# Kernel tuning notes

Hardware: AMD Instinct MI355X
Metric: run time of the kernel (lower is better)

The kernel has to match this reference:

```python
import jax, jax.numpy as jnp
import numpy as np

N_EMBD = 768
N_HEAD = 12
EPS = 1e-5

def setup_inputs() -> dict:
    key = jax.random.key(0)
    ks = jax.random.split(key, 13)
    C = N_EMBD
    s = lambda n: 1.0 / np.sqrt(n)
    return {
        "x":      jax.random.normal(ks[0], (2, 2048, C), dtype=jnp.float32),
        "ln1_w":  jnp.ones((C,), jnp.float32),
        "ln1_b":  jnp.zeros((C,), jnp.float32),
        "w_qkv":  jax.random.normal(ks[1], (C, 3 * C), dtype=jnp.float32) * s(C),
        "b_qkv":  jnp.zeros((3 * C,), jnp.float32),
        "w_proj": jax.random.normal(ks[2], (C, C), dtype=jnp.float32) * s(C),
        "b_proj": jnp.zeros((C,), jnp.float32),
        "ln2_w":  jnp.ones((C,), jnp.float32),
        "ln2_b":  jnp.zeros((C,), jnp.float32),
        "w_fc1":  jax.random.normal(ks[3], (C, 4 * C), dtype=jnp.float32) * s(C),
        "b_fc1":  jnp.zeros((4 * C,), jnp.float32),
        "w_fc2":  jax.random.normal(ks[4], (4 * C, C), dtype=jnp.float32) * s(4 * C),
        "b_fc2":  jnp.zeros((C,), jnp.float32),
    }

def _layernorm(x, w, b):
    mu = jnp.mean(x, axis=-1, keepdims=True)
    var = jnp.mean(jnp.square(x - mu), axis=-1, keepdims=True)
    return (x - mu) * jax.lax.rsqrt(var + EPS) * w + b

def reference(x, ln1_w, ln1_b, w_qkv, b_qkv, w_proj, b_proj,
              ln2_w, ln2_b, w_fc1, b_fc1, w_fc2, b_fc2):
    B, T, C = x.shape
    H = N_HEAD
    hd = C // H
    # --- attention branch ---
    h = _layernorm(x, ln1_w, ln1_b)
    qkv = h @ w_qkv + b_qkv                                  # [B,T,3C]
    q, k, v = jnp.split(qkv, 3, axis=-1)
    q = q.reshape(B, T, H, hd).transpose(0, 2, 1, 3)          # [B,H,T,hd]
    k = k.reshape(B, T, H, hd).transpose(0, 2, 1, 3)
    v = v.reshape(B, T, H, hd).transpose(0, 2, 1, 3)
    att = jnp.einsum('bhqd,bhkd->bhqk', q, k) * (1.0 / np.sqrt(hd))
    causal = jnp.tril(jnp.ones((T, T), dtype=bool))
    att = jnp.where(causal, att, -jnp.inf)
    att = jax.nn.softmax(att, axis=-1)
    y = jnp.einsum('bhqk,bhkd->bhqd', att, v)                 # [B,H,T,hd]
    y = y.transpose(0, 2, 1, 3).reshape(B, T, C)
    x = x + (y @ w_proj + b_proj)
    # --- MLP branch (dropout = identity in eval) ---
    h = _layernorm(x, ln2_w, ln2_b)
    h = jax.nn.gelu(h @ w_fc1 + b_fc1, approximate=False)
    x = x + (h @ w_fc2 + b_fc2)
    return x
```

## Files before the change

### kernel.cpp

```cpp
#include <hip/hip_runtime.h>
#include <math.h>

typedef __attribute__((ext_vector_type(8))) short short8;
typedef __attribute__((ext_vector_type(4))) float floatx4;

__device__ __forceinline__ unsigned short f2bf(float f) {
    union { float f; unsigned u; } v; v.f = f;
    unsigned r = v.u + 0x7fffu + ((v.u >> 16) & 1u);
    return (unsigned short)(r >> 16);
}

__device__ __forceinline__ float bf2f(unsigned short h) {
    union { unsigned u; float f; } v; v.u = ((unsigned)h) << 16; return v.f;
}

__device__ __forceinline__ float fexp2(float x) {
#if __has_builtin(__builtin_amdgcn_exp2f)
    return __builtin_amdgcn_exp2f(x);
#else
    return __expf(x * 0.69314718056f);
#endif
}

__device__ __forceinline__ void gload16(const unsigned short* g, unsigned short* l) {
    __builtin_amdgcn_global_load_lds(
        (const __attribute__((address_space(1))) unsigned int*)g,
        (__attribute__((address_space(3))) unsigned int*)l, 16, 0, 0);
}

__global__ __launch_bounds__(256) void ln_kernel(const float* __restrict__ x,
                                                 const float* __restrict__ w,
                                                 const float* __restrict__ b,
                                                 unsigned short* __restrict__ o) {
    int row = blockIdx.x, tid = threadIdx.x;
    const float* xr = x + (size_t)row * 768;
    float v0 = xr[tid], v1 = xr[tid + 256], v2 = xr[tid + 512];
    float s = v0 + v1 + v2, ss = v0 * v0 + v1 * v1 + v2 * v2;
#pragma unroll
    for (int o_ = 32; o_; o_ >>= 1) { s += __shfl_xor(s, o_); ss += __shfl_xor(ss, o_); }
    __shared__ float red[8];
    if ((tid & 63) == 0) { red[tid >> 6] = s; red[(tid >> 6) + 4] = ss; }
    __syncthreads();
    s = red[0] + red[1] + red[2] + red[3];
    ss = red[4] + red[5] + red[6] + red[7];
    float mu = s * (1.f / 768.f);
    float var = ss * (1.f / 768.f) - mu * mu;
    float inv = rsqrtf(var + 1e-5f);
    unsigned short* orow = o + (size_t)row * 768;
    orow[tid]       = f2bf((v0 - mu) * inv * w[tid]       + b[tid]);
    orow[tid + 256] = f2bf((v1 - mu) * inv * w[tid + 256] + b[tid + 256]);
    orow[tid + 512] = f2bf((v2 - mu) * inv * w[tid + 512] + b[tid + 512]);
}

__global__ __launch_bounds__(256) void wt_kernel(const float* __restrict__ w,
                                                 unsigned short* __restrict__ wt,
                                                 int K, int N) {
    __shared__ float t[32][33];
    int n0 = blockIdx.x * 32, k0 = blockIdx.y * 32;
    int tx = threadIdx.x & 31, ty = threadIdx.x >> 5;
#pragma unroll
    for (int i = 0; i < 32; i += 8)
        t[ty + i][tx] = w[(size_t)(k0 + ty + i) * N + n0 + tx];
    __syncthreads();
#pragma unroll
    for (int i = 0; i < 32; i += 8)
        wt[(size_t)(n0 + ty + i) * K + k0 + tx] = f2bf(t[tx][ty + i]);
}

template <int EPI>
__global__ __launch_bounds__(256) void gemm_kernel(
    const unsigned short* __restrict__ A, const unsigned short* __restrict__ Bt,
    const float* __restrict__ bias, const float* __restrict__ resid,
    float* __restrict__ fout, unsigned short* __restrict__ o0,
    unsigned short* __restrict__ o1, unsigned short* __restrict__ o2,
    int K, int Kcnt) {
    __shared__ unsigned short Al[2][128 * 32];
    __shared__ unsigned short Bl[2][128 * 32];
    int tid = threadIdx.x, lane = tid & 63, w = tid >> 6;
    int wm = w >> 1, wn = w & 1;
    int nwg = (int)(gridDim.x * gridDim.y);
    int wgid = (int)(blockIdx.y * gridDim.x + blockIdx.x);
    int logical = (wgid & 7) * (nwg >> 3) + (wgid >> 3);
    int by = logical & 31, bx = logical >> 5;
    int m0 = by * 128;
    int n0, kof = 0, chunk = 0;
    if (EPI == 4) {
        n0 = (bx % 6) * 128;
        chunk = bx / 6;
        kof = chunk * 768;
    } else {
        n0 = bx * 128;
    }
    int lr = lane & 15, lk = (lane >> 4) << 3;

    int srow = w * 32 + (lane >> 2);
    int sko = (lane & 3) << 3;
    const unsigned short* Ab = A + (size_t)(m0 + srow) * K + kof + sko;
    const unsigned short* Bb = Bt + (size_t)(n0 + srow) * K + kof + sko;

    floatx4 acc[4][4];
#pragma unroll
    for (int i = 0; i < 4; i++)
#pragma unroll
        for (int j = 0; j < 4; j++) acc[i][j] = (floatx4){0.f, 0.f, 0.f, 0.f};

    int nk = Kcnt >> 5;
    auto stage = [&](int buf, int t) {
        int k0 = t << 5;
        unsigned short* Alp = &Al[buf][(w * 32) * 32];
        unsigned short* Blp = &Bl[buf][(w * 32) * 32];
        gload16(Ab + k0, Alp);
        gload16(Ab + 16 * K + k0, Alp + 16 * 32);
        gload16(Bb + k0, Blp);
        gload16(Bb + 16 * K + k0, Blp + 16 * 32);
    };

    stage(0, 0);
    for (int t = 0; t < nk; t++) {
        int cur = t & 1;
        __syncthreads();
        if (t + 1 < nk) stage(cur ^ 1, t + 1);
        short8 af[4], bfr[4];
#pragma unroll
        for (int mt = 0; mt < 4; mt++) af[mt] = *(short8*)&Al[cur][(wm * 64 + mt * 16 + lr) * 32 + lk];
#pragma unroll
        for (int nt = 0; nt < 4; nt++) bfr[nt] = *(short8*)&Bl[cur][(wn * 64 + nt * 16 + lr) * 32 + lk];
#pragma unroll
        for (int mt = 0; mt < 4; mt++)
#pragma unroll
            for (int nt = 0; nt < 4; nt++)
                acc[mt][nt] = __builtin_amdgcn_mfma_f32_16x16x32_bf16(af[mt], bfr[nt], acc[mt][nt], 0, 0, 0);
    }

    int mb = m0 + wm * 64, nb = n0 + wn * 64;
    int sec = 0;
    if (EPI == 0) sec = n0 / 768;
#pragma unroll
    for (int mt = 0; mt < 4; mt++)
#pragma unroll
        for (int nt = 0; nt < 4; nt++)
#pragma unroll
            for (int r = 0; r < 4; r++) {
                int mrow = mb + mt * 16 + ((lane >> 4) << 2) + r;
                int ncol = nb + nt * 16 + lr;
                float val = acc[mt][nt][r];
                if (EPI != 4) val += bias[ncol];
                if (EPI == 0) {
                    int f = ncol - sec * 768;
                    int h = f >> 6, d = f & 63;
                    int bb = mrow >> 11, t = mrow & 2047;
                    if (sec == 0)
                        o0[((size_t)(bb * 12 + h) * 2048 + t) * 64 + d] = f2bf(val * 0.1803368801f);
                    else if (sec == 1)
                        o1[((size_t)(bb * 12 + h) * 2048 + t) * 64 + d] = f2bf(val);
                    else
                        o2[((size_t)(bb * 12 + h) * 64 + d) * 2048 + t] = f2bf(val);
                } else if (EPI == 1) {
                    fout[(size_t)mrow * 768 + ncol] = val + resid[(size_t)mrow * 768 + ncol];
                } else if (EPI == 2) {
                    float g = 0.5f * val * (1.f + erff(val * 0.70710678118f));
                    o0[(size_t)mrow * 3072 + ncol] = f2bf(g);
                } else if (EPI == 3) {
                    fout[(size_t)mrow * 768 + ncol] = val + resid[(size_t)mrow * 768 + ncol];
                } else {
                    unsigned short* op = (chunk == 0) ? o0 : (chunk == 1) ? o1
                                       : (chunk == 2) ? o2 : (unsigned short*)fout;
                    op[(size_t)mrow * 768 + ncol] = f2bf(val);
                }
            }
}

__global__ __launch_bounds__(256) void fc2_combine(
    const unsigned short* __restrict__ p0, const unsigned short* __restrict__ p1,
    const unsigned short* __restrict__ p2, const unsigned short* __restrict__ p3,
    const float* __restrict__ bias, const float* __restrict__ resid,
    float* __restrict__ out) {
    int i = blockIdx.x * 256 + threadIdx.x;
    size_t base = (size_t)i * 8;
    int col = (int)(base % 768);
    short8 a0 = *(const short8*)&p0[base];
    short8 a1 = *(const short8*)&p1[base];
    short8 a2 = *(const short8*)&p2[base];
    short8 a3 = *(const short8*)&p3[base];
#pragma unroll
    for (int j = 0; j < 8; j++) {
        float s = bf2f((unsigned short)a0[j]) + bf2f((unsigned short)a1[j]) +
                  bf2f((unsigned short)a2[j]) + bf2f((unsigned short)a3[j]);
        out[base + j] = s + bias[col + j] + resid[base + j];
    }
}

__global__ __launch_bounds__(256) void attn_kernel(const unsigned short* __restrict__ q_s,
                                                   const unsigned short* __restrict__ k_s,
                                                   const unsigned short* __restrict__ v_t,
                                                   unsigned short* __restrict__ y,
                                                   unsigned short* __restrict__ opart,
                                                   float* __restrict__ lpart) {
    __shared__ unsigned short KVs[2][8192];
    __shared__ unsigned short Pls[4][32][72];
    const int T = 2048, H = 12;
    int tid = threadIdx.x, lane = tid & 63, w = tid >> 6;
    int xx = (int)blockIdx.x;
    int bq, c;
    if (xx < 16)      { c = 0; bq = xx; }
    else if (xx < 28) { c = 1; bq = xx - 12; }
    else if (xx < 36) { c = 2; bq = xx - 20; }
    else              { c = 3; bq = xx - 24; }
    int bh = blockIdx.y;
    int bi = bh / H, hh = bh - bi * H;
    const unsigned short* qp = q_s + (size_t)bh * T * 64;
    const unsigned short* kp = k_s + (size_t)bh * T * 64;
    const unsigned short* vp = v_t + (size_t)bh * 64 * T;
    int wq0 = bq * 128 + w * 32;
    int lr = lane & 15, lk8 = (lane >> 4) << 3, hi = lane >> 4;
    int nt_blk = 2 * bq + 2;
    int t0 = c * 8;
    int t1 = t0 + 8 < nt_blk ? t0 + 8 : nt_blk;

    unsigned short (*Pl)[72] = Pls[w];

    int srow = tid >> 3, ssl = tid & 7;

    auto stage = [&](int buf, int t) {
        int kv0 = t * 64;
        unsigned short* base = &KVs[buf][(tid >> 6) * 512];
#pragma unroll
        for (int h = 0; h < 2; h++) {
            int r = srow + h * 32;
            int ss = ssl ^ (r & 7);
            gload16(kp + (size_t)(kv0 + r) * 64 + ss * 8, base + h * 2048);
            gload16(vp + (size_t)r * T + kv0 + ss * 8, base + 4096 + h * 2048);
        }
    };

    short8 aq[2][2];
#pragma unroll
    for (int mt = 0; mt < 2; mt++)
#pragma unroll
        for (int kf = 0; kf < 2; kf++)
            aq[mt][kf] = *(const short8*)&qp[(size_t)(wq0 + mt * 16 + lr) * 64 + kf * 32 + lk8];

    floatx4 yacc[2][4];
    float lacc[2][4];
#pragma unroll
    for (int i = 0; i < 2; i++)
#pragma unroll
        for (int j = 0; j < 4; j++) {
            yacc[i][j] = (floatx4){0.f, 0.f, 0.f, 0.f};
            lacc[i][j] = 0.f;
        }

    stage(0, t0);
    __syncthreads();

    for (int t = t0; t < t1; t++) {
        int cur = (t - t0) & 1;
        if (t + 1 < t1) stage(cur ^ 1, t + 1);
        int kv0 = t * 64;
        if (kv0 <= wq0 + 31) {
            const unsigned short* Kt = &KVs[cur][0];
            const unsigned short* Vt = &KVs[cur][4096];
            floatx4 sacc[2][4];
#pragma unroll
            for (int i = 0; i < 2; i++)
#pragma unroll
                for (int j = 0; j < 4; j++) sacc[i][j] = (floatx4){0.f, 0.f, 0.f, 0.f};
#pragma unroll
            for (int kf = 0; kf < 2; kf++) {
                int sl = ((kf << 2) | hi) ^ (lr & 7);
                short8 bk[4];
#pragma unroll
                for (int nt = 0; nt < 4; nt++)
                    bk[nt] = *(const short8*)&Kt[(nt * 16 + lr) * 64 + sl * 8];
#pragma unroll
                for (int mt = 0; mt < 2; mt++)
#pragma unroll
                    for (int nt = 0; nt < 4; nt++)
                        sacc[mt][nt] = __builtin_amdgcn_mfma_f32_16x16x32_bf16(aq[mt][kf], bk[nt], sacc[mt][nt], 0, 0, 0);
            }
            bool full = (kv0 + 63 <= wq0);
#pragma unroll
            for (int mt = 0; mt < 2; mt++)
#pragma unroll
                for (int r = 0; r < 4; r++) {
                    int qg = wq0 + mt * 16 + (hi << 2) + r;
                    int prow = mt * 16 + (hi << 2) + r;
#pragma unroll
                    for (int nt = 0; nt < 4; nt++) {
                        float sv = sacc[mt][nt][r];
                        if (!full) {
                            int kvg = kv0 + nt * 16 + lr;
                            sv = (kvg <= qg) ? sv : -1e30f;
                        }
                        float p = fexp2(sv);
                        lacc[mt][r] += p;
                        Pl[prow][nt * 16 + lr] = f2bf(p);
                    }
                }
#pragma unroll
            for (int kf = 0; kf < 2; kf++) {
                int sl = ((kf << 2) | hi) ^ (lr & 7);
                short8 pa[2], bv[4];
#pragma unroll
                for (int mt = 0; mt < 2; mt++) pa[mt] = *(short8*)&Pl[mt * 16 + lr][kf * 32 + lk8];
#pragma unroll
                for (int nt = 0; nt < 4; nt++)
                    bv[nt] = *(const short8*)&Vt[(nt * 16 + lr) * 64 + sl * 8];
#pragma unroll
                for (int mt = 0; mt < 2; mt++)
#pragma unroll
                    for (int nt = 0; nt < 4; nt++)
                        yacc[mt][nt] = __builtin_amdgcn_mfma_f32_16x16x32_bf16(pa[mt], bv[nt], yacc[mt][nt], 0, 0, 0);
            }
        }
        __syncthreads();
    }

    if (bq < 4) {
#pragma unroll
        for (int mt = 0; mt < 2; mt++)
#pragma unroll
            for (int r = 0; r < 4; r++) {
                float l = lacc[mt][r];
                l += __shfl_xor(l, 1);
                l += __shfl_xor(l, 2);
                l += __shfl_xor(l, 4);
                l += __shfl_xor(l, 8);
                float inv = 1.f / l;
                int qg = wq0 + mt * 16 + (hi << 2) + r;
#pragma unroll
                for (int nt = 0; nt < 4; nt++)
                    y[((size_t)(bi * T + qg)) * 768 + hh * 64 + nt * 16 + lr] = f2bf(yacc[mt][nt][r] * inv);
            }
    } else {
        int g = bq >> 2, rr = bq & 3;
        int base = (g == 1) ? 2 * rr : (g == 2) ? 8 + 3 * rr : 20 + 4 * rr;
        int slab = bh * 36 + base + c;
        unsigned short* op = opart + (size_t)slab * 8192;
        float* lp = lpart + (size_t)slab * 128;
#pragma unroll
        for (int mt = 0; mt < 2; mt++)
#pragma unroll
            for (int r = 0; r < 4; r++) {
                float l = lacc[mt][r];
                l += __shfl_xor(l, 1);
                l += __shfl_xor(l, 2);
                l += __shfl_xor(l, 4);
                l += __shfl_xor(l, 8);
                int wrow = w * 32 + mt * 16 + (hi << 2) + r;
                if (lr == 0) lp[wrow] = l;
#pragma unroll
                for (int nt = 0; nt < 4; nt++)
                    op[(size_t)wrow * 64 + nt * 16 + lr] = f2bf(yacc[mt][nt][r]);
            }
    }
}

__global__ __launch_bounds__(256) void attn_combine(const unsigned short* __restrict__ opart,
                                                    const float* __restrict__ lpart,
                                                    unsigned short* __restrict__ y) {
    const int T = 2048, H = 12;
    int bq = 4 + (int)blockIdx.x;
    int bh = blockIdx.y;
    int bi = bh / H, hh = bh - bi * H;
    int nchunk = (bq >> 2) + 1;
    int g = bq >> 2, rr = bq & 3;
    int base = (g == 1) ? 2 * rr : (g == 2) ? 8 + 3 * rr : 20 + 4 * rr;
    int tid = threadIdx.x;
    int row = tid >> 1, cb = (tid & 1) * 32;

    float l = 0.f;
    for (int c = 0; c < nchunk; c++) l += lpart[(size_t)(bh * 36 + base + c) * 128 + row];
    float inv = 1.f / l;

    float s[32];
#pragma unroll
    for (int j = 0; j < 32; j++) s[j] = 0.f;
    for (int c = 0; c < nchunk; c++) {
        const unsigned short* op = opart + ((size_t)(bh * 36 + base + c) * 128 + row) * 64 + cb;
#pragma unroll
        for (int v = 0; v < 4; v++) {
            short8 ob = *(const short8*)&op[v * 8];
#pragma unroll
            for (int j = 0; j < 8; j++) s[v * 8 + j] += bf2f((unsigned short)ob[j]);
        }
    }
    int qg = bq * 128 + row;
    unsigned short* yr = y + ((size_t)(bi * T + qg)) * 768 + hh * 64 + cb;
#pragma unroll
    for (int v = 0; v < 4; v++) {
        short8 ob;
#pragma unroll
        for (int j = 0; j < 8; j++) ob[j] = (short)f2bf(s[v * 8 + j] * inv);
        *(short8*)&yr[v * 8] = ob;
    }
}

extern "C" void kernel_launch(void* const* d_in, const int* in_sizes, int n_in,
                              void* d_out, int out_size, void* d_ws, size_t ws_size,
                              hipStream_t stream) {
    const float* x    = (const float*)d_in[0];
    const float* ln1w = (const float*)d_in[1];
    const float* ln1b = (const float*)d_in[2];
    const float* wqkv = (const float*)d_in[3];
    const float* bqkv = (const float*)d_in[4];
    const float* wproj= (const float*)d_in[5];
    const float* bproj= (const float*)d_in[6];
    const float* ln2w = (const float*)d_in[7];
    const float* ln2b = (const float*)d_in[8];
    const float* wfc1 = (const float*)d_in[9];
    const float* bfc1 = (const float*)d_in[10];
    const float* wfc2 = (const float*)d_in[11];
    const float* bfc2 = (const float*)d_in[12];
    float* out = (float*)d_out;

    char* ws = (char*)d_ws;
    size_t off = 0;
    auto alloc = [&](size_t bytes) { void* p = ws + off; off += (bytes + 255) & ~(size_t)255; return p; };

    const size_t MT = 4096;
    unsigned short* wqkv_t = (unsigned short*)alloc(2304 * 768 * 2);
    unsigned short* wproj_t= (unsigned short*)alloc(768 * 768 * 2);
    unsigned short* wfc1_t = (unsigned short*)alloc(3072 * 768 * 2);
    unsigned short* wfc2_t = (unsigned short*)alloc(768 * 3072 * 2);
    unsigned short* h12    = (unsigned short*)alloc(MT * 768 * 2);
    float*          x1     = (float*)alloc(MT * 768 * 4);
    unsigned short* qs     = (unsigned short*)alloc(MT * 768 * 2);
    unsigned short* ks     = (unsigned short*)alloc(MT * 768 * 2);
    unsigned short* vt     = (unsigned short*)alloc(MT * 768 * 2);
    unsigned short* yb     = (unsigned short*)alloc(MT * 768 * 2);
    unsigned short* hm     = qs;
    unsigned short* opart  = (unsigned short*)alloc(24 * 36 * 8192 * 2);
    float*          lpart  = (float*)alloc(24 * 36 * 128 * 4);

    unsigned short* p0 = (unsigned short*)ws;
    unsigned short* p1 = opart;
    unsigned short* p2 = (unsigned short*)((char*)opart + (size_t)MT * 768 * 2);
    unsigned short* p3 = h12;

    wt_kernel<<<dim3(2304 / 32, 768 / 32), 256, 0, stream>>>(wqkv, wqkv_t, 768, 2304);
    wt_kernel<<<dim3(768 / 32, 768 / 32), 256, 0, stream>>>(wproj, wproj_t, 768, 768);
    wt_kernel<<<dim3(3072 / 32, 768 / 32), 256, 0, stream>>>(wfc1, wfc1_t, 768, 3072);
    wt_kernel<<<dim3(768 / 32, 3072 / 32), 256, 0, stream>>>(wfc2, wfc2_t, 3072, 768);

    ln_kernel<<<4096, 256, 0, stream>>>(x, ln1w, ln1b, h12);
    gemm_kernel<0><<<dim3(18, 32), 256, 0, stream>>>(h12, wqkv_t, bqkv, nullptr, nullptr, qs, ks, vt, 768, 768);
    attn_kernel<<<dim3(40, 24), 256, 0, stream>>>(qs, ks, vt, yb, opart, lpart);
    attn_combine<<<dim3(12, 24), 256, 0, stream>>>(opart, lpart, yb);
    gemm_kernel<1><<<dim3(6, 32), 256, 0, stream>>>(yb, wproj_t, bproj, x, x1, nullptr, nullptr, nullptr, 768, 768);
    ln_kernel<<<4096, 256, 0, stream>>>(x1, ln2w, ln2b, h12);
    gemm_kernel<2><<<dim3(24, 32), 256, 0, stream>>>(h12, wfc1_t, bfc1, nullptr, nullptr, hm, nullptr, nullptr, 768, 768);
    gemm_kernel<4><<<dim3(24, 32), 256, 0, stream>>>(hm, wfc2_t, nullptr, nullptr, (float*)p3, p0, p1, p2, 3072, 768);
    fc2_combine<<<dim3(1536), 256, 0, stream>>>(p0, p1, p2, p3, bfc2, x1, out);
}
```

Baseline: 215.8 us.

## Use 256x128 tiles with 512-thread blocks for QKV, FC1 and split-K FC2 GEMMs

```diff
diff --git a/kernel.cpp b/kernel.cpp
--- a/kernel.cpp
+++ b/kernel.cpp
@@ -82,21 +82,13 @@
     int wgid = (int)(blockIdx.y * gridDim.x + blockIdx.x);
     int logical = (wgid & 7) * (nwg >> 3) + (wgid >> 3);
     int by = logical & 31, bx = logical >> 5;
-    int m0 = by * 128;
-    int n0, kof = 0, chunk = 0;
-    if (EPI == 4) {
-        n0 = (bx % 6) * 128;
-        chunk = bx / 6;
-        kof = chunk * 768;
-    } else {
-        n0 = bx * 128;
-    }
+    int m0 = by * 128, n0 = bx * 128;
     int lr = lane & 15, lk = (lane >> 4) << 3;
 
     int srow = w * 32 + (lane >> 2);
     int sko = (lane & 3) << 3;
-    const unsigned short* Ab = A + (size_t)(m0 + srow) * K + kof + sko;
-    const unsigned short* Bb = Bt + (size_t)(n0 + srow) * K + kof + sko;
+    const unsigned short* Ab = A + (size_t)(m0 + srow) * K + sko;
+    const unsigned short* Bb = Bt + (size_t)(n0 + srow) * K + sko;
 
     floatx4 acc[4][4];
 #pragma unroll
@@ -113,6 +105,84 @@
         gload16(Ab + 16 * K + k0, Alp + 16 * 32);
         gload16(Bb + k0, Blp);
         gload16(Bb + 16 * K + k0, Blp + 16 * 32);
+    };
+
+    stage(0, 0);
+    for (int t = 0; t < nk; t++) {
+        int cur = t & 1;
+        __syncthreads();
+        if (t + 1 < nk) stage(cur ^ 1, t + 1);
+        short8 af[4], bfr[4];
+#pragma unroll
+        for (int mt = 0; mt < 4; mt++) af[mt] = *(short8*)&Al[cur][(wm * 64 + mt * 16 + lr) * 32 + lk];
+#pragma unroll
+        for (int nt = 0; nt < 4; nt++) bfr[nt] = *(short8*)&Bl[cur][(wn * 64 + nt * 16 + lr) * 32 + lk];
+#pragma unroll
+        for (int mt = 0; mt < 4; mt++)
+#pragma unroll
+            for (int nt = 0; nt < 4; nt++)
+                acc[mt][nt] = __builtin_amdgcn_mfma_f32_16x16x32_bf16(af[mt], bfr[nt], acc[mt][nt], 0, 0, 0);
+    }
+
+    int mb = m0 + wm * 64, nb = n0 + wn * 64;
+#pragma unroll
+    for (int mt = 0; mt < 4; mt++)
+#pragma unroll
+        for (int nt = 0; nt < 4; nt++)
+#pragma unroll
+            for (int r = 0; r < 4; r++) {
+                int mrow = mb + mt * 16 + ((lane >> 4) << 2) + r;
+                int ncol = nb + nt * 16 + lr;
+                float val = acc[mt][nt][r] + bias[ncol];
+                fout[(size_t)mrow * 768 + ncol] = val + resid[(size_t)mrow * 768 + ncol];
+            }
+}
+
+template <int EPI>
+__global__ __launch_bounds__(512) void gemm256_kernel(
+    const unsigned short* __restrict__ A, const unsigned short* __restrict__ Bt,
+    const float* __restrict__ bias, const float* __restrict__ resid,
+    float* __restrict__ fout, unsigned short* __restrict__ o0,
+    unsigned short* __restrict__ o1, unsigned short* __restrict__ o2,
+    int K, int Kcnt) {
+    __shared__ unsigned short Al[2][256 * 32];
+    __shared__ unsigned short Bl[2][128 * 32];
+    int tid = threadIdx.x, lane = tid & 63, w = tid >> 6;
+    int wm = w >> 1, wn = w & 1;
+    int nwg = (int)(gridDim.x * gridDim.y);
+    int wgid = (int)(blockIdx.y * gridDim.x + blockIdx.x);
+    int logical = (wgid & 7) * (nwg >> 3) + (wgid >> 3);
+    int my = (int)gridDim.y;
+    int by = logical % my, bx = logical / my;
+    int m0 = by * 256;
+    int n0, kof = 0, chunk = 0;
+    if (EPI == 4) {
+        n0 = (bx % 6) * 128;
+        chunk = bx / 6;
+        kof = chunk * 768;
+    } else {
+        n0 = bx * 128;
+    }
+    int lr = lane & 15, lk = (lane >> 4) << 3;
+
+    int arow = w * 32 + (lane >> 2);
+    int brow = w * 16 + (lane >> 2);
+    int sko = (lane & 3) << 3;
+    const unsigned short* Ab = A + (size_t)(m0 + arow) * K + kof + sko;
+    const unsigned short* Bb = Bt + (size_t)(n0 + brow) * K + kof + sko;
+
+    floatx4 acc[4][4];
+#pragma unroll
+    for (int i = 0; i < 4; i++)
+#pragma unroll
+        for (int j = 0; j < 4; j++) acc[i][j] = (floatx4){0.f, 0.f, 0.f, 0.f};
+
+    int nk = Kcnt >> 5;
+    auto stage = [&](int buf, int t) {
+        int k0 = t << 5;
+        gload16(Ab + k0, &Al[buf][(w * 32) * 32]);
+        gload16(Ab + 16 * K + k0, &Al[buf][(w * 32 + 16) * 32]);
+        gload16(Bb + k0, &Bl[buf][(w * 16) * 32]);
     };
 
     stage(0, 0);
@@ -155,13 +225,9 @@
                         o1[((size_t)(bb * 12 + h) * 2048 + t) * 64 + d] = f2bf(val);
                     else
                         o2[((size_t)(bb * 12 + h) * 64 + d) * 2048 + t] = f2bf(val);
-                } else if (EPI == 1) {
-                    fout[(size_t)mrow * 768 + ncol] = val + resid[(size_t)mrow * 768 + ncol];
                 } else if (EPI == 2) {
                     float g = 0.5f * val * (1.f + erff(val * 0.70710678118f));
                     o0[(size_t)mrow * 3072 + ncol] = f2bf(g);
-                } else if (EPI == 3) {
-                    fout[(size_t)mrow * 768 + ncol] = val + resid[(size_t)mrow * 768 + ncol];
                 } else {
                     unsigned short* op = (chunk == 0) ? o0 : (chunk == 1) ? o1
                                        : (chunk == 2) ? o2 : (unsigned short*)fout;
@@ -444,12 +510,12 @@
     wt_kernel<<<dim3(768 / 32, 3072 / 32), 256, 0, stream>>>(wfc2, wfc2_t, 3072, 768);
 
     ln_kernel<<<4096, 256, 0, stream>>>(x, ln1w, ln1b, h12);
-    gemm_kernel<0><<<dim3(18, 32), 256, 0, stream>>>(h12, wqkv_t, bqkv, nullptr, nullptr, qs, ks, vt, 768, 768);
+    gemm256_kernel<0><<<dim3(18, 16), 512, 0, stream>>>(h12, wqkv_t, bqkv, nullptr, nullptr, qs, ks, vt, 768, 768);
     attn_kernel<<<dim3(40, 24), 256, 0, stream>>>(qs, ks, vt, yb, opart, lpart);
     attn_combine<<<dim3(12, 24), 256, 0, stream>>>(opart, lpart, yb);
     gemm_kernel<1><<<dim3(6, 32), 256, 0, stream>>>(yb, wproj_t, bproj, x, x1, nullptr, nullptr, nullptr, 768, 768);
     ln_kernel<<<4096, 256, 0, stream>>>(x1, ln2w, ln2b, h12);
-    gemm_kernel<2><<<dim3(24, 32), 256, 0, stream>>>(h12, wfc1_t, bfc1, nullptr, nullptr, hm, nullptr, nullptr, 768, 768);
-    gemm_kernel<4><<<dim3(24, 32), 256, 0, stream>>>(hm, wfc2_t, nullptr, nullptr, (float*)p3, p0, p1, p2, 3072, 768);
+    gemm256_kernel<2><<<dim3(24, 16), 512, 0, stream>>>(h12, wfc1_t, bfc1, nullptr, nullptr, hm, nullptr, nullptr, 768, 768);
+    gemm256_kernel<4><<<dim3(24, 16), 512, 0, stream>>>(hm, wfc2_t, nullptr, nullptr, (float*)p3, p0, p1, p2, 3072, 768);
     fc2_combine<<<dim3(1536), 256, 0, stream>>>(p0, p1, p2, p3, bfc2, x1, out);
 }
```

Result: slower. 229.0 us (+6.1%).

## Load V fragments directly from global in attention and merge weight-transpose launches

Applied to the files above, without the earlier changes.

```diff
diff --git a/kernel.cpp b/kernel.cpp
--- a/kernel.cpp
+++ b/kernel.cpp
@@ -52,11 +52,19 @@
     orow[tid + 512] = f2bf((v2 - mu) * inv * w[tid + 512] + b[tid + 512]);
 }
 
-__global__ __launch_bounds__(256) void wt_kernel(const float* __restrict__ w,
-                                                 unsigned short* __restrict__ wt,
-                                                 int K, int N) {
+__global__ __launch_bounds__(256) void wt_all_kernel(
+    const float* __restrict__ w0, unsigned short* __restrict__ t0,
+    const float* __restrict__ w1, unsigned short* __restrict__ t1,
+    const float* __restrict__ w2, unsigned short* __restrict__ t2,
+    const float* __restrict__ w3, unsigned short* __restrict__ t3) {
+    int bid = (int)blockIdx.x;
+    const float* w; unsigned short* wt; int K, N, bx, by;
+    if (bid < 1728)      { w = w0; wt = t0; K = 768;  N = 2304; int l = bid;        bx = l % 72; by = l / 72; }
+    else if (bid < 2304) { w = w1; wt = t1; K = 768;  N = 768;  int l = bid - 1728; bx = l % 24; by = l / 24; }
+    else if (bid < 4608) { w = w2; wt = t2; K = 768;  N = 3072; int l = bid - 2304; bx = l % 96; by = l / 96; }
+    else                 { w = w3; wt = t3; K = 3072; N = 768;  int l = bid - 4608; bx = l % 24; by = l / 24; }
     __shared__ float t[32][33];
-    int n0 = blockIdx.x * 32, k0 = blockIdx.y * 32;
+    int n0 = bx * 32, k0 = by * 32;
     int tx = threadIdx.x & 31, ty = threadIdx.x >> 5;
 #pragma unroll
     for (int i = 0; i < 32; i += 8)
@@ -160,8 +168,6 @@
                 } else if (EPI == 2) {
                     float g = 0.5f * val * (1.f + erff(val * 0.70710678118f));
                     o0[(size_t)mrow * 3072 + ncol] = f2bf(g);
-                } else if (EPI == 3) {
-                    fout[(size_t)mrow * 768 + ncol] = val + resid[(size_t)mrow * 768 + ncol];
                 } else {
                     unsigned short* op = (chunk == 0) ? o0 : (chunk == 1) ? o1
                                        : (chunk == 2) ? o2 : (unsigned short*)fout;
@@ -196,7 +202,7 @@
                                                    unsigned short* __restrict__ y,
                                                    unsigned short* __restrict__ opart,
                                                    float* __restrict__ lpart) {
-    __shared__ unsigned short KVs[2][8192];
+    __shared__ unsigned short KVs[2][4096];
     __shared__ unsigned short Pls[4][32][72];
     const int T = 2048, H = 12;
     int tid = threadIdx.x, lane = tid & 63, w = tid >> 6;
@@ -229,7 +235,6 @@
             int r = srow + h * 32;
             int ss = ssl ^ (r & 7);
             gload16(kp + (size_t)(kv0 + r) * 64 + ss * 8, base + h * 2048);
-            gload16(vp + (size_t)r * T + kv0 + ss * 8, base + 4096 + h * 2048);
         }
     };
 
@@ -259,7 +264,6 @@
         int kv0 = t * 64;
         if (kv0 <= wq0 + 31) {
             const unsigned short* Kt = &KVs[cur][0];
-            const unsigned short* Vt = &KVs[cur][4096];
             floatx4 sacc[2][4];
 #pragma unroll
             for (int i = 0; i < 2; i++)
@@ -278,6 +282,12 @@
                     for (int nt = 0; nt < 4; nt++)
                         sacc[mt][nt] = __builtin_amdgcn_mfma_f32_16x16x32_bf16(aq[mt][kf], bk[nt], sacc[mt][nt], 0, 0, 0);
             }
+            short8 bv[4][2];
+#pragma unroll
+            for (int nt = 0; nt < 4; nt++)
+#pragma unroll
+                for (int kf = 0; kf < 2; kf++)
+                    bv[nt][kf] = *(const short8*)&vp[(size_t)(nt * 16 + lr) * T + kv0 + kf * 32 + lk8];
             bool full = (kv0 + 63 <= wq0);
 #pragma unroll
             for (int mt = 0; mt < 2; mt++)
@@ -299,18 +309,14 @@
                 }
 #pragma unroll
             for (int kf = 0; kf < 2; kf++) {
-                int sl = ((kf << 2) | hi) ^ (lr & 7);
-                short8 pa[2], bv[4];
+                short8 pa[2];
 #pragma unroll
                 for (int mt = 0; mt < 2; mt++) pa[mt] = *(short8*)&Pl[mt * 16 + lr][kf * 32 + lk8];
 #pragma unroll
-                for (int nt = 0; nt < 4; nt++)
-                    bv[nt] = *(const short8*)&Vt[(nt * 16 + lr) * 64 + sl * 8];
-#pragma unroll
                 for (int mt = 0; mt < 2; mt++)
 #pragma unroll
                     for (int nt = 0; nt < 4; nt++)
-                        yacc[mt][nt] = __builtin_amdgcn_mfma_f32_16x16x32_bf16(pa[mt], bv[nt], yacc[mt][nt], 0, 0, 0);
+                        yacc[mt][nt] = __builtin_amdgcn_mfma_f32_16x16x32_bf16(pa[mt], bv[nt][kf], yacc[mt][nt], 0, 0, 0);
             }
         }
         __syncthreads();
@@ -438,10 +444,8 @@
     unsigned short* p2 = (unsigned short*)((char*)opart + (size_t)MT * 768 * 2);
     unsigned short* p3 = h12;
 
-    wt_kernel<<<dim3(2304 / 32, 768 / 32), 256, 0, stream>>>(wqkv, wqkv_t, 768, 2304);
-    wt_kernel<<<dim3(768 / 32, 768 / 32), 256, 0, stream>>>(wproj, wproj_t, 768, 768);
-    wt_kernel<<<dim3(3072 / 32, 768 / 32), 256, 0, stream>>>(wfc1, wfc1_t, 768, 3072);
-    wt_kernel<<<dim3(768 / 32, 3072 / 32), 256, 0, stream>>>(wfc2, wfc2_t, 3072, 768);
+    wt_all_kernel<<<dim3(6912), 256, 0, stream>>>(wqkv, wqkv_t, wproj, wproj_t,
+                                                  wfc1, wfc1_t, wfc2, wfc2_t);
 
     ln_kernel<<<4096, 256, 0, stream>>>(x, ln1w, ln1b, h12);
     gemm_kernel<0><<<dim3(18, 32), 256, 0, stream>>>(h12, wqkv_t, bqkv, nullptr, nullptr, qs, ks, vt, 768, 768);
```

Result: no change. 211.9 us (-1.8%).
